# Kernel optimization log

Measured on AMD Instinct MI355X. Metric: run time of the kernel, lower is better.

## Reference

```python
import jax, jax.numpy as jnp
import numpy as np

R, M1, N1, M2, N2 = 4, 1024, 2048, 2, 4
BATCH, SEQ = 4, 2048


def setup_inputs() -> dict:
    key = jax.random.key(0)
    k_x, k_A, k_B, k_b, k_p, k_q = jax.random.split(key, 6)
    x = jax.random.normal(k_x, (BATCH, SEQ, M1 * M2), dtype=jnp.float32)
    A = jax.random.normal(k_A, (R, N1, M1), dtype=jnp.float32) * 0.001
    B = jax.random.normal(k_B, (R, M2, N2), dtype=jnp.float32) * 0.001
    b = jnp.zeros((N1 * N2,), dtype=jnp.float32)
    p_inv = jax.random.permutation(k_p, M1 * M2).astype(jnp.int32)
    q = jax.random.permutation(k_q, N1 * N2).astype(jnp.int32)
    return {"x": x, "A": A, "B": B, "b": b, "p_inv": p_inv, "q": q}


def reference(x, A, B, b, p_inv, q):
    # x: [Bt, S, m1*m2]; A: [r, n1, m1]; B: [r, m2, n2]
    r, n1, m1 = A.shape
    _, m2, n2 = B.shape
    shape = x.shape
    tokens = shape[0] * shape[1]
    # input permutation gather (use_p=True)
    xp = x[:, :, p_inv]
    # Bx = einsum('km,rmn->rkn'): [r, tokens*m1, n2]
    xf = xp.reshape(-1, m2)
    Bx = jnp.einsum('km,rmn->rkn', xf, B)
    Bx = Bx.reshape(r, tokens, m1, n2)
    # ABx = einsum('rnm,rbmj->bnj'): [tokens, n1, n2]
    ABx = jnp.einsum('rnm,rbmj->bnj', A, Bx)
    ABx = ABx.reshape(shape[:-1] + (n1 * n2,))
    # output permutation gather (use_q=True) + bias
    out = ABx[:, :, q] + b
    return out
```

## Files before the change

kernel.cpp:

```cpp
#include <hip/hip_runtime.h>
#include <hip/hip_bf16.h>

typedef unsigned short u16;
typedef __attribute__((ext_vector_type(8))) short short8;
typedef __attribute__((ext_vector_type(4))) float floatx4;

#define TOKENS 8192
#define KDIM   2048
#define NFEAT  8192
#define R_     4
#define N1_    2048
#define M1_    1024

#define BM 256
#define BN 256
#define BK 64
#define NKT (KDIM / BK)

__device__ __forceinline__ u16 f2bf(float f) {
  union { float f; unsigned u; } v; v.f = f;
  unsigned r = v.u + 0x7fffu + ((v.u >> 16) & 1u);
  return (u16)(r >> 16);
}

#define CVT_BLOCKS 16384
struct u16x4 { u16 a, b, c, d; };
__global__ void k_prep(const float4* __restrict__ x4, u16x4* __restrict__ xb,
                       const float* __restrict__ A, const float* __restrict__ Bm,
                       const int* __restrict__ p_inv, const int* __restrict__ q,
                       u16* __restrict__ Wf) {
  __shared__ int pfs[KDIM];
  int bid = blockIdx.x;
  if (bid < CVT_BLOCKS) {
    int i = bid * 256 + threadIdx.x;
    float4 v = x4[i];
    u16x4 o; o.a = f2bf(v.x); o.b = f2bf(v.y); o.c = f2bf(v.z); o.d = f2bf(v.w);
    xb[i] = o;
  } else {
    int f = bid - CVT_BLOCKS;
    for (int i = threadIdx.x; i < KDIM; i += 256) pfs[p_inv[i]] = i;
    __syncthreads();
    int k0 = threadIdx.x * 8;
    int qf = q[f];
    int n = qf >> 2, jq = qf & 3;
    const float* An = A + (size_t)n * M1_;
    float bc[8];
#pragma unroll
    for (int r = 0; r < R_; ++r) {
      bc[r * 2 + 0] = Bm[r * 8 + 0 * 4 + jq];
      bc[r * 2 + 1] = Bm[r * 8 + 1 * 4 + jq];
    }
    u16 w[8];
#pragma unroll
    for (int i = 0; i < 8; ++i) {
      int c = pfs[k0 + i];
      int m1 = c >> 1, m2 = c & 1;
      float acc = 0.f;
#pragma unroll
      for (int r = 0; r < R_; ++r)
        acc += An[(size_t)r * (N1_ * M1_) + m1] * bc[r * 2 + m2];
      w[i] = f2bf(acc);
    }
    *(short8*)(Wf + (size_t)f * KDIM + k0) = *(const short8*)w;
  }
}

#define GLD16(gp, lp) __builtin_amdgcn_global_load_lds( \
    (const __attribute__((address_space(1))) void*)(gp), \
    (__attribute__((address_space(3))) void*)(lp), 16, 0, 0)

#define FENCE asm volatile("" ::: "memory")
#define BAR   do { FENCE; __builtin_amdgcn_s_barrier(); FENCE; } while (0)
#define VMCNT(n) asm volatile("s_waitcnt vmcnt(" #n ")" ::: "memory")

__global__ __launch_bounds__(512, 2) void k_gemm(
    const u16* __restrict__ X, const u16* __restrict__ W,
    const float* __restrict__ bias, float* __restrict__ out) {
  __shared__ __align__(16) char lds[2 * 65536];

  int bid = blockIdx.x;
  int xcd = bid & 7;
  int loc = bid >> 3;
  int u = loc >> 5, v = loc & 31;
  int tM = xcd * 4 + (v >> 3);
  int tN = u * 8 + (v & 7);
  int rowBase = tM * BM, colBase = tN * BN;

  int tid = threadIdx.x, lane = tid & 63, wave = tid >> 6;
  int wm = wave >> 2;
  int wn = wave & 3;

  int srow = tid >> 3;
  int scol = ((tid & 7) ^ (srow & 7)) * 8;
  const u16* Asrc = X + (size_t)(rowBase + srow) * KDIM + scol;
  const u16* Bsrc = W + (size_t)(colBase + srow) * KDIM + scol;

  auto SA = [&](int slot, int half, int kt) {
#pragma unroll
    for (int jj = 0; jj < 2; ++jj)
      GLD16(Asrc + (size_t)(half * 128 + jj * 64) * KDIM + kt * 64,
            &lds[slot * 65536 + half * 16384 + jj * 8192 + tid * 16]);
  };
  auto SB = [&](int slot, int half, int kt) {
#pragma unroll
    for (int jj = 0; jj < 2; ++jj)
      GLD16(Bsrc + (size_t)(half * 128 + jj * 64) * KDIM + kt * 64,
            &lds[slot * 65536 + 32768 + half * 16384 + jj * 8192 + tid * 16]);
  };

  int l15 = lane & 15, lhi = lane >> 4, l7 = lane & 7;
  int x0 = (lhi ^ l7) * 16;
  int x1 = ((4 + lhi) ^ l7) * 16;
  int abase = wm * 16384 + l15 * 128;
  int bbase = 32768 + (wn >> 1) * 16384 + ((wn & 1) * 64 + l15) * 128;

  auto RA = [&](int slot, int m, int kk) -> short8 {
    return *(const short8*)&lds[slot * 65536 + abase + m * 2048 + (kk ? x1 : x0)];
  };
  auto RB = [&](int slot, int n, int kk) -> short8 {
    return *(const short8*)&lds[slot * 65536 + bbase + n * 2048 + (kk ? x1 : x0)];
  };

  floatx4 acc[8][4] = {};

  auto PHASE = [&](int cs, int t, bool full) {
    if (full) {
      SA(cs ^ 1, 0, t + 1); SA(cs ^ 1, 1, t + 1);
      SB(cs ^ 1, 0, t + 1); SB(cs ^ 1, 1, t + 1);
    }
    short8 af[8], bf[4];
#pragma unroll
    for (int m = 0; m < 8; ++m) af[m] = RA(cs, m, 0);
#pragma unroll
    for (int n = 0; n < 4; ++n) bf[n] = RB(cs, n, 0);
    __builtin_amdgcn_s_setprio(1);
#pragma unroll
    for (int m = 0; m < 8; ++m)
#pragma unroll
      for (int n = 0; n < 4; ++n)
        acc[m][n] = __builtin_amdgcn_mfma_f32_16x16x32_bf16(af[m], bf[n], acc[m][n], 0, 0, 0);
    __builtin_amdgcn_s_setprio(0);
#pragma unroll
    for (int m = 0; m < 8; ++m) af[m] = RA(cs, m, 1);
#pragma unroll
    for (int n = 0; n < 4; ++n) bf[n] = RB(cs, n, 1);
    __builtin_amdgcn_s_setprio(1);
#pragma unroll
    for (int m = 0; m < 8; ++m)
#pragma unroll
      for (int n = 0; n < 4; ++n)
        acc[m][n] = __builtin_amdgcn_mfma_f32_16x16x32_bf16(af[m], bf[n], acc[m][n], 0, 0, 0);
    __builtin_amdgcn_s_setprio(0);
    if (full) { VMCNT(0); BAR; }
  };

  SA(0, 0, 0); SA(0, 1, 0); SB(0, 0, 0); SB(0, 1, 0);
  VMCNT(0); BAR;

#pragma unroll 1
  for (int it = 0; it < NKT / 2; ++it) {
    PHASE(0, 2 * it, true);
    PHASE(1, 2 * it + 1, 2 * it + 1 < NKT - 1);
  }

  float bv[4];
#pragma unroll
  for (int n = 0; n < 4; ++n)
    bv[n] = bias[colBase + wn * 64 + n * 16 + l15];
#pragma unroll
  for (int m = 0; m < 8; ++m) {
    int r0 = wm * 128 + m * 16 + (lhi << 2);
#pragma unroll
    for (int n = 0; n < 4; ++n) {
      size_t basep = (size_t)(rowBase + r0) * NFEAT + colBase + wn * 64 + n * 16 + l15;
#pragma unroll
      for (int reg = 0; reg < 4; ++reg)
        out[basep + (size_t)reg * NFEAT] = acc[m][n][reg] + bv[n];
    }
  }
}

extern "C" void kernel_launch(void* const* d_in, const int* in_sizes, int n_in,
                              void* d_out, int out_size, void* d_ws, size_t ws_size,
                              hipStream_t stream) {
  const float* x     = (const float*)d_in[0];
  const float* A     = (const float*)d_in[1];
  const float* Bm    = (const float*)d_in[2];
  const float* bias  = (const float*)d_in[3];
  const int*   p_inv = (const int*)d_in[4];
  const int*   q     = (const int*)d_in[5];
  float* out = (float*)d_out;

  u16* Xb = (u16*)d_ws;
  u16* Wf = (u16*)((char*)d_ws + (size_t)TOKENS * KDIM * 2);

  k_prep<<<CVT_BLOCKS + NFEAT, 256, 0, stream>>>((const float4*)x, (u16x4*)Xb, A, Bm, p_inv, q, Wf);
  k_gemm<<<(TOKENS / BM) * (NFEAT / BN), 512, 0, stream>>>(Xb, Wf, bias, out);
}
```

Measured before the change: 327.5 us.

## Restructure GEMM into 256x128 tiles with triple-buffered LDS and register prefetch

The GEMM tile shrinks from 256x256 with 8 waves to 256x128 with 4 waves, and the K step drops from 64 to 32. The LDS moves from two buffers to a three-slot ring, so global loads run two k-steps ahead. The next step's fragments are read from LDS into alternate register sets while the current MFMAs issue. The aim is to hide global and LDS latency behind the MFMAs instead of draining all loads before each barrier. The cost is a smaller tile with lower reuse per block, more blocks, and more barriers per unit of work.

```diff
diff --git a/kernel.cpp b/kernel.cpp
--- a/kernel.cpp
+++ b/kernel.cpp
@@ -13,9 +13,10 @@
 #define M1_    1024
 
 #define BM 256
-#define BN 256
-#define BK 64
+#define BN 128
+#define BK 32
 #define NKT (KDIM / BK)
+#define SLOT 24576
 
 __device__ __forceinline__ u16 f2bf(float f) {
   union { float f; unsigned u; } v; v.f = f;
@@ -71,12 +72,13 @@
 
 #define FENCE asm volatile("" ::: "memory")
 #define BAR   do { FENCE; __builtin_amdgcn_s_barrier(); FENCE; } while (0)
+#define LGKM0 asm volatile("s_waitcnt lgkmcnt(0)" ::: "memory")
 #define VMCNT(n) asm volatile("s_waitcnt vmcnt(" #n ")" ::: "memory")
 
-__global__ __launch_bounds__(512, 2) void k_gemm(
+__global__ __launch_bounds__(256, 2) void k_gemm(
     const u16* __restrict__ X, const u16* __restrict__ W,
     const float* __restrict__ bias, float* __restrict__ out) {
-  __shared__ __align__(16) char lds[2 * 65536];
+  __shared__ __align__(16) char lds[3 * SLOT];
 
   int bid = blockIdx.x;
   int xcd = bid & 7;
@@ -87,81 +89,89 @@
   int rowBase = tM * BM, colBase = tN * BN;
 
   int tid = threadIdx.x, lane = tid & 63, wave = tid >> 6;
-  int wm = wave >> 2;
-  int wn = wave & 3;
-
-  int srow = tid >> 3;
-  int scol = ((tid & 7) ^ (srow & 7)) * 8;
-  const u16* Asrc = X + (size_t)(rowBase + srow) * KDIM + scol;
-  const u16* Bsrc = W + (size_t)(colBase + srow) * KDIM + scol;
-
-  auto SA = [&](int slot, int half, int kt) {
+  int wm = wave >> 1, wn = wave & 1;
+
+  int sr = tid >> 2;
+  int sc = ((tid & 3) ^ (sr & 3)) * 8;
+  const u16* Asrc = X + (size_t)(rowBase + sr) * KDIM + sc;
+  const u16* Bsrc = W + (size_t)(colBase + sr) * KDIM + sc;
+
+  auto STAGE = [&](unsigned sb, int t) {
+    int ks = t * BK;
+#pragma unroll
+    for (int jj = 0; jj < 4; ++jj)
+      GLD16(Asrc + (size_t)jj * 64 * KDIM + ks, &lds[sb + jj * 4096 + tid * 16]);
 #pragma unroll
     for (int jj = 0; jj < 2; ++jj)
-      GLD16(Asrc + (size_t)(half * 128 + jj * 64) * KDIM + kt * 64,
-            &lds[slot * 65536 + half * 16384 + jj * 8192 + tid * 16]);
-  };
-  auto SB = [&](int slot, int half, int kt) {
-#pragma unroll
-    for (int jj = 0; jj < 2; ++jj)
-      GLD16(Bsrc + (size_t)(half * 128 + jj * 64) * KDIM + kt * 64,
-            &lds[slot * 65536 + 32768 + half * 16384 + jj * 8192 + tid * 16]);
-  };
-
-  int l15 = lane & 15, lhi = lane >> 4, l7 = lane & 7;
-  int x0 = (lhi ^ l7) * 16;
-  int x1 = ((4 + lhi) ^ l7) * 16;
-  int abase = wm * 16384 + l15 * 128;
-  int bbase = 32768 + (wn >> 1) * 16384 + ((wn & 1) * 64 + l15) * 128;
-
-  auto RA = [&](int slot, int m, int kk) -> short8 {
-    return *(const short8*)&lds[slot * 65536 + abase + m * 2048 + (kk ? x1 : x0)];
-  };
-  auto RB = [&](int slot, int n, int kk) -> short8 {
-    return *(const short8*)&lds[slot * 65536 + bbase + n * 2048 + (kk ? x1 : x0)];
-  };
+      GLD16(Bsrc + (size_t)jj * 64 * KDIM + ks, &lds[sb + 16384 + jj * 4096 + tid * 16]);
+  };
+
+  int l15 = lane & 15, lhi = lane >> 4;
+  int sx = (lhi ^ (lane & 3)) * 16;
+  int aoff = (wm * 128 + l15) * 64 + sx;
+  int boff = 16384 + (wn * 64 + l15) * 64 + sx;
 
   floatx4 acc[8][4] = {};
-
-  auto PHASE = [&](int cs, int t, bool full) {
-    if (full) {
-      SA(cs ^ 1, 0, t + 1); SA(cs ^ 1, 1, t + 1);
-      SB(cs ^ 1, 0, t + 1); SB(cs ^ 1, 1, t + 1);
-    }
-    short8 af[8], bf[4];
-#pragma unroll
-    for (int m = 0; m < 8; ++m) af[m] = RA(cs, m, 0);
-#pragma unroll
-    for (int n = 0; n < 4; ++n) bf[n] = RB(cs, n, 0);
+  short8 aE[8], bE[4], aO[8], bO[4];
+
+  auto RDE = [&](unsigned sb) {
+#pragma unroll
+    for (int m = 0; m < 8; ++m) aE[m] = *(const short8*)&lds[sb + aoff + m * 1024];
+#pragma unroll
+    for (int n = 0; n < 4; ++n) bE[n] = *(const short8*)&lds[sb + boff + n * 1024];
+  };
+  auto RDO = [&](unsigned sb) {
+#pragma unroll
+    for (int m = 0; m < 8; ++m) aO[m] = *(const short8*)&lds[sb + aoff + m * 1024];
+#pragma unroll
+    for (int n = 0; n < 4; ++n) bO[n] = *(const short8*)&lds[sb + boff + n * 1024];
+  };
+
+  auto MME = [&]() {
     __builtin_amdgcn_s_setprio(1);
 #pragma unroll
     for (int m = 0; m < 8; ++m)
 #pragma unroll
       for (int n = 0; n < 4; ++n)
-        acc[m][n] = __builtin_amdgcn_mfma_f32_16x16x32_bf16(af[m], bf[n], acc[m][n], 0, 0, 0);
+        acc[m][n] = __builtin_amdgcn_mfma_f32_16x16x32_bf16(aE[m], bE[n], acc[m][n], 0, 0, 0);
     __builtin_amdgcn_s_setprio(0);
-#pragma unroll
-    for (int m = 0; m < 8; ++m) af[m] = RA(cs, m, 1);
-#pragma unroll
-    for (int n = 0; n < 4; ++n) bf[n] = RB(cs, n, 1);
+  };
+  auto MMO = [&]() {
     __builtin_amdgcn_s_setprio(1);
 #pragma unroll
     for (int m = 0; m < 8; ++m)
 #pragma unroll
       for (int n = 0; n < 4; ++n)
-        acc[m][n] = __builtin_amdgcn_mfma_f32_16x16x32_bf16(af[m], bf[n], acc[m][n], 0, 0, 0);
+        acc[m][n] = __builtin_amdgcn_mfma_f32_16x16x32_bf16(aO[m], bO[n], acc[m][n], 0, 0, 0);
     __builtin_amdgcn_s_setprio(0);
-    if (full) { VMCNT(0); BAR; }
-  };
-
-  SA(0, 0, 0); SA(0, 1, 0); SB(0, 0, 0); SB(0, 1, 0);
-  VMCNT(0); BAR;
-
+  };
+
+  STAGE(0, 0); STAGE(SLOT, 1); STAGE(2 * SLOT, 2);
+  VMCNT(6); BAR;
+  RDE(0);
+
+  unsigned sb0 = 0, sb1 = SLOT, sb2 = 2 * SLOT;
 #pragma unroll 1
-  for (int it = 0; it < NKT / 2; ++it) {
-    PHASE(0, 2 * it, true);
-    PHASE(1, 2 * it + 1, 2 * it + 1 < NKT - 1);
+  for (int t = 0; t < NKT - 2; t += 2) {
+    LGKM0;
+    STAGE(sb0, t + 3);
+    RDO(sb1);
+    MME();
+    VMCNT(6);
+    BAR;
+    LGKM0;
+    if (t < NKT - 4) STAGE(sb1, t + 4);
+    RDE(sb2);
+    MMO();
+    if (t < NKT - 4) { VMCNT(6); } else { VMCNT(0); }
+    BAR;
+    unsigned tmp = sb0; sb0 = sb2; sb2 = sb1; sb1 = tmp;
   }
+  LGKM0;
+  RDO(sb1);
+  MME();
+  LGKM0;
+  MMO();
 
   float bv[4];
 #pragma unroll
@@ -195,5 +205,5 @@
   u16* Wf = (u16*)((char*)d_ws + (size_t)TOKENS * KDIM * 2);
 
   k_prep<<<CVT_BLOCKS + NFEAT, 256, 0, stream>>>((const float4*)x, (u16x4*)Xb, A, Bm, p_inv, q, Wf);
-  k_gemm<<<(TOKENS / BM) * (NFEAT / BN), 512, 0, stream>>>(Xb, Wf, bias, out);
-}
+  k_gemm<<<(TOKENS / BM) * (NFEAT / BN), 256, 0, stream>>>(Xb, Wf, bias, out);
+}
```

New measurement: 352.1 us. 1.08x slower.
